# Optimization experiments

Hardware: AMD Instinct MI355X
Metric: run time of the kernel (lower is better)

The kernel has to match this reference:

```python
import jax, jax.numpy as jnp
import numpy as np

NEG_INF = -1e12
ALPHA = 0.01  # LeakyReLU slope


def setup_inputs() -> dict:
    key = jax.random.key(0)
    ks = jax.random.split(key, 12)
    K, N, DIN, H1, DOUT, FC1 = 64, 1024, 16, 4, 8, 54
    X = jax.random.normal(ks[0], (K, N, DIN), dtype=jnp.float32)
    adj = jax.random.randint(ks[1], (N, N), 0, 2, dtype=jnp.int32)
    # Xavier-uniform-ish init scale (gain 1.414)
    def xavier(k, shape):
        fan_in, fan_out = shape[0], shape[-1]
        lim = 1.414 * np.sqrt(6.0 / (fan_in + fan_out))
        return jax.random.uniform(k, shape, jnp.float32, -lim, lim)
    W1 = xavier(ks[2], (DIN, H1))
    a1 = xavier(ks[3], (2 * H1, 1))
    W2 = xavier(ks[4], (H1, DOUT))
    a2 = xavier(ks[5], (2 * DOUT, 1))
    fc1_w = xavier(ks[6], (N * DOUT, FC1))
    fc1_b = jnp.zeros((FC1,), jnp.float32)
    out_w = xavier(ks[7], (FC1, N))
    out_b = jnp.zeros((N,), jnp.float32)
    return {"X": X, "adj": adj, "W1": W1, "a1": a1, "W2": W2, "a2": a2,
            "fc1_w": fc1_w, "fc1_b": fc1_b, "out_w": out_w, "out_b": out_b}


def _gat_layer(h_in, adj, W, a):
    # h: [K, N, F]
    h = jnp.matmul(h_in, W)
    Fdim = W.shape[1]
    # concat(h_i, h_j) @ a  ==  (h_i . a[:F]) + (h_j . a[F:])
    f1 = jnp.matmul(h, a[:Fdim, 0])  # [K, N]
    f2 = jnp.matmul(h, a[Fdim:, 0])  # [K, N]
    e = jax.nn.leaky_relu(f1[:, :, None] + f2[:, None, :], ALPHA)  # [K, N, N]
    e = jnp.where(adj[None, :, :] > 0, e, NEG_INF)
    att = jax.nn.softmax(e, axis=2)
    return jnp.einsum('kij,kjf->kif', att, h)


def reference(X, adj, W1, a1, W2, a2, fc1_w, fc1_b, out_w, out_b):
    x = jax.nn.relu(_gat_layer(X, adj, W1, a1))
    x = jax.nn.relu(_gat_layer(x, adj, W2, a2))
    x = x.reshape(x.shape[0], -1)  # [K, N*dim_output]
    x = jax.nn.relu(jnp.matmul(x, fc1_w) + fc1_b)
    return jnp.matmul(x, out_w) + out_b  # [K, N] q-values
```

## Files before the change

### kernel.cpp

```cpp
#include <hip/hip_runtime.h>
#include <hip/hip_bf16.h>

constexpr int K    = 64;
constexpr int N    = 1024;
constexpr int DIN  = 16;
constexpr int H1   = 4;
constexpr int DOUT = 8;
constexpr int FC1  = 54;

#define ALPHA_F   (0.01f)
#define LOG2E_F   (1.4426950408889634f)

typedef unsigned int uint;
typedef short  bf16x8 __attribute__((ext_vector_type(8)));
typedef float  f32x4  __attribute__((ext_vector_type(4)));

__device__ inline float fast_exp2(float x) {
#if __has_builtin(__builtin_amdgcn_exp2f)
    return __builtin_amdgcn_exp2f(x);
#else
    return __expf(x * 0.6931471805599453f);
#endif
}

__device__ inline uint pk_bf16(float a, float b) {
    union { __hip_bfloat162 h; uint u; } v;
    v.h = __float22bfloat162_rn(make_float2(a, b));
    return v.u;
}


__global__ __launch_bounds__(512) void prep_kernel(
        const int* __restrict__ adj, unsigned long long* __restrict__ maskM,
        const float* __restrict__ fc1w, float* __restrict__ wt,
        const float* __restrict__ X, const float* __restrict__ W1,
        const float* __restrict__ a1,
        uint4* __restrict__ HB1, float* __restrict__ f11, float* __restrict__ f21) {
    int b = blockIdx.x;
    if (b < 2048) {
        int wave = threadIdx.x >> 6, lane = threadIdx.x & 63;
        int wid = b * 8 + wave;
        int jw  = wid >> 10;
        int i   = wid & 1023;
        int v = adj[i * N + (jw << 6) + lane];
        unsigned long long m = __ballot(v > 0);
        if (lane == 0) maskM[i * 16 + jw] = m;
    } else if (b < 2112) {
        __shared__ float tile[128 * FC1];
        const int m0 = (b - 2048) * 128;
        const float* src = fc1w + (size_t)m0 * FC1;
        for (int idx = threadIdx.x; idx < 128 * FC1; idx += 512)
            tile[idx] = src[idx];
        __syncthreads();
        for (int idx = threadIdx.x; idx < 128 * FC1; idx += 512) {
            int c = idx >> 7, mm = idx & 127;
            wt[(size_t)c * (N * DOUT) + m0 + mm] = tile[mm * FC1 + c];
        }
    } else {
        __shared__ float hrow[512 * 4];
        const int bb  = b - 2112;
        const int k   = bb >> 1;
        const int j0  = (bb & 1) * 512;
        const int tid = threadIdx.x;
        const int idx = k * N + j0 + tid;
        const float4* x4 = (const float4*)(X + (size_t)idx * DIN);
        float hv_[H1] = {0.f, 0.f, 0.f, 0.f};
        #pragma unroll
        for (int q = 0; q < 4; q++) {
            float4 xv = x4[q];
            #pragma unroll
            for (int f = 0; f < H1; f++) {
                hv_[f] += xv.x * W1[(q * 4 + 0) * H1 + f] + xv.y * W1[(q * 4 + 1) * H1 + f]
                        + xv.z * W1[(q * 4 + 2) * H1 + f] + xv.w * W1[(q * 4 + 3) * H1 + f];
            }
        }
        float s1 = 0.f, s2 = 0.f;
        #pragma unroll
        for (int f = 0; f < H1; f++) { s1 += hv_[f] * a1[f]; s2 += hv_[f] * a1[H1 + f]; }
        f11[idx] = s1 * LOG2E_F;
        f21[idx] = s2 * LOG2E_F;
        #pragma unroll
        for (int f = 0; f < H1; f++) hrow[tid * 4 + f] = hv_[f];
        __syncthreads();
        uint4* HBk = HB1 + (size_t)k * 2048 + (j0 >> 5) * 64;
        #pragma unroll
        for (int e = tid; e < 1024; e += 512) {
            int cl = e >> 6, l = e & 63, q = (l >> 4), n = l & 15;
            uint4 dw;
            if (n < H1) {
                const float* hp = hrow + (cl * 32 + q * 8) * 4 + n;
                dw.x = pk_bf16(hp[0],  hp[4]);
                dw.y = pk_bf16(hp[8],  hp[12]);
                dw.z = pk_bf16(hp[16], hp[20]);
                dw.w = pk_bf16(hp[24], hp[28]);
            } else if (n == H1) {
                dw = make_uint4(0x3f803f80u, 0x3f803f80u, 0x3f803f80u, 0x3f803f80u);
            } else {
                dw = make_uint4(0u, 0u, 0u, 0u);
            }
            HBk[cl * 64 + l] = dw;
        }
    }
}

template <int F, bool FUSE>
__global__ __launch_bounds__(512, 4) void gat_attn_mfma(
        const unsigned long long* __restrict__ maskM,
        const uint4* __restrict__ HBin,
        const float* __restrict__ f1,
        const float* __restrict__ f2,
        const float* __restrict__ W2,
        const float* __restrict__ a2,
        uint4* __restrict__ HBout,
        float* __restrict__ o_x,
        float* __restrict__ o_f1,
        float* __restrict__ o_f2) {
    __shared__ float F2s[1024];
    __shared__ float XPa[8][16][5];
    __shared__ float XPb[8][16][9];

    const int tid  = threadIdx.x;
    const int lane = tid & 63;
    const int wv   = tid >> 6;
    const int quad = lane >> 4;
    const int n16  = lane & 15;
    const int k    = blockIdx.x >> 3;

    if (tid < 256)
        ((float4*)F2s)[tid] = ((const float4*)(f2 + k * N))[tid];
    __syncthreads();

    const int itile = (blockIdx.x & 7) * 8 + wv;
    const int ibase = itile * 16;
    const int irow  = ibase + n16;
    const float f1v = f1[k * N + irow];
    const uint4* mrow = (const uint4*)((const char*)maskM + (size_t)irow * 128);
    const uint4* HBk  = HBin + (size_t)k * 2048;

    f32x4 acc = {0.f, 0.f, 0.f, 0.f};
    union { bf16x8 v; uint u[4]; } af;
    union { bf16x8 v; uint4 q; }  bfrag;

    #pragma unroll 2
    for (int g = 0; g < 8; g++) {
        const uint4 Mg = mrow[g];
        #pragma unroll
        for (int cc = 0; cc < 4; cc++) {
            const int c = g * 4 + cc;
            const uint mdw = (cc == 0) ? Mg.x : (cc == 1) ? Mg.y
                           : (cc == 2) ? Mg.z : Mg.w;
            const uint mb  = (mdw >> (quad * 8)) & 0xffu;
            float4 fa = *(const float4*)(F2s + c * 32 + quad * 8);
            float4 fb = *(const float4*)(F2s + c * 32 + quad * 8 + 4);
            bfrag.q = HBk[c * 64 + lane];
            float f2e[8] = {fa.x, fa.y, fa.z, fa.w, fb.x, fb.y, fb.z, fb.w};
            float pv[8];
            #pragma unroll
            for (int jj = 0; jj < 8; jj++) {
                float x = f1v + f2e[jj];
                float e = fmaxf(x, ALPHA_F * x);
                float p = fast_exp2(e);
                pv[jj] = (mb & (1u << jj)) ? p : 0.f;
            }
            #pragma unroll
            for (int pr = 0; pr < 4; pr++)
                af.u[pr] = pk_bf16(pv[2 * pr], pv[2 * pr + 1]);
            acc = __builtin_amdgcn_mfma_f32_16x16x32_bf16(af.v, bfrag.v, acc, 0, 0, 0);
        }
    }

    #pragma unroll
    for (int r = 0; r < 4; r++) {
        float den = __shfl(acc[r], (lane & 48) + F);
        float inv = (den > 0.f) ? 1.f / den : 0.f;
        float xo  = fmaxf(acc[r] * inv, 0.f);
        int m = quad * 4 + r;
        if constexpr (FUSE) {
            if (n16 < F) XPa[wv][m][n16] = xo;
        } else {
            if (n16 < F) o_x[((size_t)k * N + ibase + m) * F + n16] = xo;
        }
    }

    if constexpr (FUSE) {
        __syncthreads();
        if (lane < 16) {
            const int m = lane;
            float x0 = XPa[wv][m][0], x1 = XPa[wv][m][1];
            float x2v = XPa[wv][m][2], x3 = XPa[wv][m][3];
            float hv[DOUT];
            #pragma unroll
            for (int f = 0; f < DOUT; f++) {
                hv[f] = x0 * W2[f]      + x1 * W2[8 + f]
                      + x2v * W2[16 + f] + x3 * W2[24 + f];
            }
            float t1 = 0.f, t2 = 0.f;
            #pragma unroll
            for (int f = 0; f < DOUT; f++) { t1 += hv[f] * a2[f]; t2 += hv[f] * a2[DOUT + f]; }
            const int row = k * N + ibase + m;
            o_f1[row] = t1 * LOG2E_F;
            o_f2[row] = t2 * LOG2E_F;
            #pragma unroll
            for (int f = 0; f < DOUT; f++) XPb[wv][m][f] = hv[f];
        }
        __syncthreads();
        if (lane < 32) {
            const int c2    = ibase >> 5;
            const int qhalf = (ibase >> 4) & 1;
            const int ql    = lane >> 4;
            const int n     = lane & 15;
            const int q     = qhalf * 2 + ql;
            uint4 dw;
            if (n < DOUT) {
                dw.x = pk_bf16(XPb[wv][ql * 8 + 0][n], XPb[wv][ql * 8 + 1][n]);
                dw.y = pk_bf16(XPb[wv][ql * 8 + 2][n], XPb[wv][ql * 8 + 3][n]);
                dw.z = pk_bf16(XPb[wv][ql * 8 + 4][n], XPb[wv][ql * 8 + 5][n]);
                dw.w = pk_bf16(XPb[wv][ql * 8 + 6][n], XPb[wv][ql * 8 + 7][n]);
            } else if (n == DOUT) {
                dw = make_uint4(0x3f803f80u, 0x3f803f80u, 0x3f803f80u, 0x3f803f80u);
            } else {
                dw = make_uint4(0u, 0u, 0u, 0u);
            }
            HBout[(size_t)k * 2048 + c2 * 64 + q * 16 + n] = dw;
        }
    }
}

__global__ __launch_bounds__(256) void fc1_kernel(
        const float* __restrict__ x2, const float* __restrict__ wt,
        const float* __restrict__ b, float* __restrict__ y) {
    const int bid  = blockIdx.x;
    const int k    = bid / FC1;
    const int c    = bid - k * FC1;
    const int wave = threadIdx.x >> 6;
    const int lane = threadIdx.x & 63;
    const float4* x4 = (const float4*)(x2 + (size_t)k * N * DOUT) + wave * 512 + lane;
    const float4* w4 = (const float4*)(wt + (size_t)c * N * DOUT) + wave * 512 + lane;
    float s0 = 0.f, s1 = 0.f;
    #pragma unroll
    for (int q = 0; q < 8; q += 2) {
        float4 a0 = x4[q * 64],      w0 = w4[q * 64];
        float4 a1 = x4[q * 64 + 64], w1 = w4[q * 64 + 64];
        s0 += a0.x * w0.x + a0.y * w0.y + a0.z * w0.z + a0.w * w0.w;
        s1 += a1.x * w1.x + a1.y * w1.y + a1.z * w1.z + a1.w * w1.w;
    }
    float s = s0 + s1;
    #pragma unroll
    for (int off = 32; off > 0; off >>= 1) s += __shfl_xor(s, off);
    __shared__ float red[4];
    if (lane == 0) red[wave] = s;
    __syncthreads();
    if (threadIdx.x == 0)
        y[bid] = fmaxf(red[0] + red[1] + red[2] + red[3] + b[c], 0.f);
}

__global__ void fc2_kernel(const float* __restrict__ y,
                           const float* __restrict__ out_w,
                           const float* __restrict__ out_b,
                           float* __restrict__ out) {
    int n = blockIdx.x * blockDim.x + threadIdx.x;
    int k = blockIdx.y;
    const float* yk = y + (size_t)k * FC1;
    float s = out_b[n];
    #pragma unroll 6
    for (int c = 0; c < FC1; c++) s += yk[c] * out_w[(size_t)c * N + n];
    out[(size_t)k * N + n] = s;
}

extern "C" void kernel_launch(void* const* d_in, const int* in_sizes, int n_in,
                              void* d_out, int out_size, void* d_ws, size_t ws_size,
                              hipStream_t stream) {
    const float* X     = (const float*)d_in[0];
    const int*   adj   = (const int*)  d_in[1];
    const float* W1    = (const float*)d_in[2];
    const float* a1    = (const float*)d_in[3];
    const float* W2    = (const float*)d_in[4];
    const float* a2    = (const float*)d_in[5];
    const float* fc1w  = (const float*)d_in[6];
    const float* fc1b  = (const float*)d_in[7];
    const float* outw  = (const float*)d_in[8];
    const float* outb  = (const float*)d_in[9];
    float* out = (float*)d_out;

    float* ws  = (float*)d_ws;
    float* f11 = ws;
    float* f21 = f11 + 65536;
    float* f12 = f21 + 65536;
    float* f22 = f12 + 65536;
    float* x2  = f22 + 65536;
    float* y   = x2  + 524288;
    float* wt  = y   + 4096;
    unsigned long long* mM = (unsigned long long*)(wt + 442368);
    uint4* HB1 = (uint4*)(wt + 442368 + 32768);
    uint4* HB2 = HB1 + 131072;

    prep_kernel<<<dim3(2240), dim3(512), 0, stream>>>(
        adj, mM, fc1w, wt, X, W1, a1, HB1, f11, f21);

    gat_attn_mfma<4, true><<<dim3(K * 8), dim3(512), 0, stream>>>(
        mM, HB1, f11, f21, W2, a2, HB2, nullptr, f12, f22);

    gat_attn_mfma<8, false><<<dim3(K * 8), dim3(512), 0, stream>>>(
        mM, HB2, f12, f22, nullptr, nullptr, nullptr, x2, nullptr, nullptr);

    fc1_kernel<<<dim3(K * FC1), dim3(256), 0, stream>>>(x2, wt, fc1b, y);
    fc2_kernel<<<dim3(N / 256, K), dim3(256), 0, stream>>>(y, outw, outb, out);
}
```

Baseline: 134.7 us.

## Tile fc1 over row chunks with shared-memory weights, drop fc1 weight transpose

Removes the fc1 weight transpose from the prep kernel and rewrites fc1 as a split-K tiled GEMM. Each block loads a 256-row slice of fc1_w and 8 batch rows of activations into shared memory and writes partial sums. fc2 now reduces those 32 partials, adds the bias and ReLU, then applies the output layer. This cuts prep work and lets weights be reused across batch rows, at the cost of an extra partial-sum buffer and a larger reduction inside fc2.

```diff
diff --git a/kernel.cpp b/kernel.cpp
--- a/kernel.cpp
+++ b/kernel.cpp
@@ -32,7 +32,6 @@
 
 __global__ __launch_bounds__(512) void prep_kernel(
         const int* __restrict__ adj, unsigned long long* __restrict__ maskM,
-        const float* __restrict__ fc1w, float* __restrict__ wt,
         const float* __restrict__ X, const float* __restrict__ W1,
         const float* __restrict__ a1,
         uint4* __restrict__ HB1, float* __restrict__ f11, float* __restrict__ f21) {
@@ -45,20 +44,9 @@
         int v = adj[i * N + (jw << 6) + lane];
         unsigned long long m = __ballot(v > 0);
         if (lane == 0) maskM[i * 16 + jw] = m;
-    } else if (b < 2112) {
-        __shared__ float tile[128 * FC1];
-        const int m0 = (b - 2048) * 128;
-        const float* src = fc1w + (size_t)m0 * FC1;
-        for (int idx = threadIdx.x; idx < 128 * FC1; idx += 512)
-            tile[idx] = src[idx];
-        __syncthreads();
-        for (int idx = threadIdx.x; idx < 128 * FC1; idx += 512) {
-            int c = idx >> 7, mm = idx & 127;
-            wt[(size_t)c * (N * DOUT) + m0 + mm] = tile[mm * FC1 + c];
-        }
     } else {
         __shared__ float hrow[512 * 4];
-        const int bb  = b - 2112;
+        const int bb  = b - 2048;
         const int k   = bb >> 1;
         const int j0  = (bb & 1) * 512;
         const int tid = threadIdx.x;
@@ -227,43 +215,76 @@
 }
 
 __global__ __launch_bounds__(256) void fc1_kernel(
-        const float* __restrict__ x2, const float* __restrict__ wt,
-        const float* __restrict__ b, float* __restrict__ y) {
-    const int bid  = blockIdx.x;
-    const int k    = bid / FC1;
-    const int c    = bid - k * FC1;
-    const int wave = threadIdx.x >> 6;
-    const int lane = threadIdx.x & 63;
-    const float4* x4 = (const float4*)(x2 + (size_t)k * N * DOUT) + wave * 512 + lane;
-    const float4* w4 = (const float4*)(wt + (size_t)c * N * DOUT) + wave * 512 + lane;
-    float s0 = 0.f, s1 = 0.f;
+        const float* __restrict__ x2, const float* __restrict__ fc1w,
+        float* __restrict__ yp) {
+    __shared__ float ws[256 * FC1];
+    __shared__ float xs[8 * 256];
+    const int t  = threadIdx.x;
+    const int bx = blockIdx.x;
+    const int kt = bx & 7;
+    const int s  = bx >> 3;
+    const int m0 = s << 8;
+    const int k0 = kt << 3;
+
+    const float4* wsrc = (const float4*)(fc1w + (size_t)m0 * FC1);
+    float4* ws4 = (float4*)ws;
     #pragma unroll
-    for (int q = 0; q < 8; q += 2) {
-        float4 a0 = x4[q * 64],      w0 = w4[q * 64];
-        float4 a1 = x4[q * 64 + 64], w1 = w4[q * 64 + 64];
-        s0 += a0.x * w0.x + a0.y * w0.y + a0.z * w0.z + a0.w * w0.w;
-        s1 += a1.x * w1.x + a1.y * w1.y + a1.z * w1.z + a1.w * w1.w;
-    }
-    float s = s0 + s1;
+    for (int i = t; i < (256 * FC1) / 4; i += 256) ws4[i] = wsrc[i];
+
+    {
+        float4* xs4 = (float4*)xs;
+        const int r = t >> 6, col = t & 63;
+        #pragma unroll
+        for (int rr = 0; rr < 8; rr += 4)
+            xs4[(r + rr) * 64 + col] =
+                ((const float4*)(x2 + (size_t)(k0 + r + rr) * (N * DOUT) + m0))[col];
+    }
+    __syncthreads();
+
+    const int c    = t & 63;
+    const int kq   = t >> 6;
+    const int ceff = (c < FC1) ? c : 0;
+    const float* xa = xs + (kq * 2) * 256;
+    const float* xb = xa + 256;
+    float acc0 = 0.f, acc1 = 0.f;
+    #pragma unroll 8
+    for (int m = 0; m < 256; m++) {
+        float w = ws[m * FC1 + ceff];
+        acc0 += w * xa[m];
+        acc1 += w * xb[m];
+    }
+    float* yrow = yp + ((size_t)s * 64 + k0 + kq * 2) * 64 + c;
+    yrow[0]  = acc0;
+    yrow[64] = acc1;
+}
+
+__global__ __launch_bounds__(512) void fc2_kernel(
+        const float* __restrict__ yp, const float* __restrict__ fc1b,
+        const float* __restrict__ outw, const float* __restrict__ outb,
+        float* __restrict__ out) {
+    __shared__ float red[512];
+    __shared__ float ybuf[FC1];
+    const int t = threadIdx.x;
+    const int k = blockIdx.y;
+    const int c = t & 63, sg = t >> 6;
+    float v = 0.f;
     #pragma unroll
-    for (int off = 32; off > 0; off >>= 1) s += __shfl_xor(s, off);
-    __shared__ float red[4];
-    if (lane == 0) red[wave] = s;
+    for (int j = 0; j < 4; j++)
+        v += yp[((size_t)(sg + 8 * j) * 64 + k) * 64 + c];
+    red[t] = v;
     __syncthreads();
-    if (threadIdx.x == 0)
-        y[bid] = fmaxf(red[0] + red[1] + red[2] + red[3] + b[c], 0.f);
-}
-
-__global__ void fc2_kernel(const float* __restrict__ y,
-                           const float* __restrict__ out_w,
-                           const float* __restrict__ out_b,
-                           float* __restrict__ out) {
-    int n = blockIdx.x * blockDim.x + threadIdx.x;
-    int k = blockIdx.y;
-    const float* yk = y + (size_t)k * FC1;
-    float s = out_b[n];
+    if (t < FC1) {
+        float s = fc1b[t];
+        #pragma unroll
+        for (int g = 0; g < 8; g++) s += red[g * 64 + t];
+        ybuf[t] = fmaxf(s, 0.f);
+    }
+    __syncthreads();
+    const int n = blockIdx.x * 512 + t;
+    float s = outb[n];
     #pragma unroll 6
-    for (int c = 0; c < FC1; c++) s += yk[c] * out_w[(size_t)c * N + n];
+    for (int cc = 0; cc < FC1; cc++)
+        s += ybuf[cc] * outw[(size_t)cc * N + n];
     out[(size_t)k * N + n] = s;
 }
 
@@ -288,14 +309,13 @@
     float* f12 = f21 + 65536;
     float* f22 = f12 + 65536;
     float* x2  = f22 + 65536;
-    float* y   = x2  + 524288;
-    float* wt  = y   + 4096;
-    unsigned long long* mM = (unsigned long long*)(wt + 442368);
-    uint4* HB1 = (uint4*)(wt + 442368 + 32768);
+    float* yp  = x2  + 524288;
+    unsigned long long* mM = (unsigned long long*)(yp + 131072);
+    uint4* HB1 = (uint4*)(yp + 131072 + 32768);
     uint4* HB2 = HB1 + 131072;
 
-    prep_kernel<<<dim3(2240), dim3(512), 0, stream>>>(
-        adj, mM, fc1w, wt, X, W1, a1, HB1, f11, f21);
+    prep_kernel<<<dim3(2176), dim3(512), 0, stream>>>(
+        adj, mM, X, W1, a1, HB1, f11, f21);
 
     gat_attn_mfma<4, true><<<dim3(K * 8), dim3(512), 0, stream>>>(
         mM, HB1, f11, f21, W2, a2, HB2, nullptr, f12, f22);
@@ -303,6 +323,7 @@
     gat_attn_mfma<8, false><<<dim3(K * 8), dim3(512), 0, stream>>>(
         mM, HB2, f12, f22, nullptr, nullptr, nullptr, x2, nullptr, nullptr);
 
-    fc1_kernel<<<dim3(K * FC1), dim3(256), 0, stream>>>(x2, wt, fc1b, y);
-    fc2_kernel<<<dim3(N / 256, K), dim3(256), 0, stream>>>(y, outw, outb, out);
-}
+    fc1_kernel<<<dim3(256), dim3(256), 0, stream>>>(x2, fc1w, yp);
+
+    fc2_kernel<<<dim3(2, K), dim3(512), 0, stream>>>(yp, fc1b, outw, outb, out);
+}
```

After: 132.1 us. About the same (-1.9%).
